# Kernel optimization log

Hardware: AMD Instinct MI355X
Metric: run time of the kernel (lower is better)

## Reference

```python
import jax, jax.numpy as jnp
import numpy as np

D_MODEL = 2048
N_HEADS = 16
GKV = 4
D_FF = 8192
D_HEAD = D_MODEL // N_HEADS
EPS = 1e-6


def rmsnorm(x, w):
    ms = jnp.mean(x * x, axis=-1, keepdims=True)
    return x * jax.lax.rsqrt(ms + EPS) * w


def attention(q, k, v, mask=None):
    # q: (B,Tq,H,d), k/v: (B,Tk,H,d)
    scale = 1.0 / jnp.sqrt(jnp.asarray(q.shape[-1], q.dtype))
    scores = jnp.einsum('bqhd,bkhd->bhqk', q, k) * scale
    if mask is not None:
        scores = scores + mask
    probs = jax.nn.softmax(scores, axis=-1)
    return jnp.einsum('bhqk,bkhd->bqhd', probs, v)


def setup_inputs() -> dict:
    key = jax.random.key(0)
    ks = jax.random.split(key, 12)
    B, T = 2, 2048
    s = 0.02
    return {
        'x': jax.random.normal(ks[0], (B, T, D_MODEL), jnp.float32),
        'k_ctx': jax.random.normal(ks[1], (B, T, GKV, D_HEAD), jnp.float32),
        'v_ctx': jax.random.normal(ks[2], (B, T, GKV, D_HEAD), jnp.float32),
        # cross-attn params (weights stored as (in, out); y = x @ W)
        'wq': jax.random.normal(ks[3], (D_MODEL, D_MODEL), jnp.float32) * s,
        'wo_cross': jax.random.normal(ks[4], (D_MODEL, D_MODEL), jnp.float32) * s,
        'norm_q_w': jnp.ones((D_MODEL,), jnp.float32),
        # self-attn params
        'wqkv': jax.random.normal(ks[5], (D_MODEL, 3 * D_MODEL), jnp.float32) * s,
        'wo_self': jax.random.normal(ks[6], (D_MODEL, D_MODEL), jnp.float32) * s,
        'norm_qkv_w': jnp.ones((D_MODEL,), jnp.float32),
        # FFN params (bias=False in FeedForward)
        'ffn_w1': jax.random.normal(ks[7], (D_MODEL, D_FF), jnp.float32) * s,
        'ffn_w2': jax.random.normal(ks[8], (D_FF, D_MODEL), jnp.float32) * s,
        'ffn_norm_w': jnp.ones((D_MODEL,), jnp.float32),
    }


def reference(x, k_ctx, v_ctx, wq, wo_cross, norm_q_w, wqkv, wo_self,
              norm_qkv_w, ffn_w1, ffn_w2, ffn_norm_w):
    B, T, D = x.shape
    repeat = N_HEADS // GKV

    # ---- cross attention (GQA) ----
    q = (rmsnorm(x, norm_q_w) @ wq).reshape(B, T, N_HEADS, D_HEAD)
    k = jnp.repeat(k_ctx, repeat, axis=2)  # (B,Tk,H,d), matches repeat_interleave
    v = jnp.repeat(v_ctx, repeat, axis=2)
    ctx = attention(q, k, v, mask=None).reshape(B, T, D)
    x = x + ctx @ wo_cross

    # ---- causal self attention ----
    xn = rmsnorm(x, norm_qkv_w)
    qkv = xn @ wqkv
    qs, ks_, vs = jnp.split(qkv, 3, axis=-1)
    qs = qs.reshape(B, T, N_HEADS, D_HEAD)
    ks_ = ks_.reshape(B, T, N_HEADS, D_HEAD)
    vs = vs.reshape(B, T, N_HEADS, D_HEAD)
    causal_mask = jnp.triu(jnp.full((T, T), -jnp.inf, x.dtype), k=1)[None, None]
    ctx2 = attention(qs, ks_, vs, mask=causal_mask).reshape(B, T, D)
    x = x + ctx2 @ wo_self

    # ---- FFN (SiLU) ----
    h = rmsnorm(x, ffn_norm_w)
    y = jax.nn.silu(h @ ffn_w1) @ ffn_w2
    return x + y
```

## Files before the change

kernel.cpp:

```cpp
#include <hip/hip_runtime.h>
#include <math.h>

typedef unsigned short u16;
typedef __attribute__((ext_vector_type(4))) u16 u16x4;
typedef __attribute__((ext_vector_type(8))) u16 u16x8;
typedef __attribute__((ext_vector_type(8))) __bf16 bf16x8;
typedef __attribute__((ext_vector_type(4))) float f32x4;
typedef __attribute__((ext_vector_type(16))) float f32x16;
typedef __attribute__((ext_vector_type(4))) unsigned u32x4;

#define D_MODEL 2048
#define SEQ 2048
#define BATCH 2
#define NH 16
#define HD 128
#define DFF 8192
#define ROWS (BATCH * SEQ)

__device__ __forceinline__ u16 f2bf(float f) {
  union { float f; unsigned u; } v; v.f = f;
  unsigned r = v.u + 0x7FFFu + ((v.u >> 16) & 1u);
  return (u16)(r >> 16);
}
__device__ __forceinline__ u16 to_bf16(float f) { return f2bf(f); }
__device__ __forceinline__ u16 to_bf16(u16 v) { return v; }

__device__ __forceinline__ f32x4 mfma16(u16x8 a, u16x8 b, f32x4 c) {
  return __builtin_amdgcn_mfma_f32_16x16x32_bf16(
      __builtin_bit_cast(bf16x8, a), __builtin_bit_cast(bf16x8, b), c, 0, 0, 0);
}
__device__ __forceinline__ f32x16 mfma32(u16x8 a, u16x8 b, f32x16 c) {
  return __builtin_amdgcn_mfma_f32_32x32x16_bf16(
      __builtin_bit_cast(bf16x8, a), __builtin_bit_cast(bf16x8, b), c, 0, 0, 0);
}

__device__ __forceinline__ void gll16(const void* g, void* l) {
  __builtin_amdgcn_global_load_lds(
      (const __attribute__((address_space(1))) void*)g,
      (__attribute__((address_space(3))) void*)l, 16, 0, 0);
}

__global__ __launch_bounds__(256) void cast_kernel(const float* __restrict__ in,
                                                   u16* __restrict__ out, int n8) {
  int i = blockIdx.x * 256 + threadIdx.x;
  if (i >= n8) return;
  const float4* p = (const float4*)in + (size_t)i * 2;
  float4 a = p[0], b = p[1];
  u16x8 o;
  o[0] = f2bf(a.x); o[1] = f2bf(a.y); o[2] = f2bf(a.z); o[3] = f2bf(a.w);
  o[4] = f2bf(b.x); o[5] = f2bf(b.y); o[6] = f2bf(b.z); o[7] = f2bf(b.w);
  *((u16x8*)out + i) = o;
}

__global__ __launch_bounds__(256) void cast_transpose_kernel(
    const float* __restrict__ in, u16* __restrict__ out, int K, int N) {
  __shared__ float tile[64][65];
  int n0 = blockIdx.x * 64, k0 = blockIdx.y * 64;
  int tx = threadIdx.x & 63, ty = threadIdx.x >> 6;
#pragma unroll
  for (int i = 0; i < 64; i += 4)
    tile[ty + i][tx] = in[(size_t)(k0 + ty + i) * N + n0 + tx];
  __syncthreads();
#pragma unroll
  for (int i = 0; i < 64; i += 4)
    out[(size_t)(n0 + ty + i) * K + k0 + tx] = f2bf(tile[tx][ty + i]);
}

template <typename ST>
__global__ __launch_bounds__(256) void build_vt_kernel(
    const ST* __restrict__ src, u16* __restrict__ dst, int HZ,
    size_t src_b_stride, size_t src_h_stride, int src_tok_stride) {
  __shared__ u16 tl[64][72];
  int z = blockIdx.z, zb = z / HZ, zh = z % HZ;
  const ST* s = src + (size_t)zb * src_b_stride + (size_t)zh * src_h_stride;
  int t0 = blockIdx.x * 64, d0 = blockIdx.y * 64;
  int rr = threadIdx.x >> 4, cc = (threadIdx.x & 15) * 4;
#pragma unroll
  for (int pp = 0; pp < 4; ++pp) {
    int t = pp * 16 + rr;
    const ST* sp = s + (size_t)(t0 + t) * src_tok_stride + d0 + cc;
#pragma unroll
    for (int j = 0; j < 4; ++j) tl[t][cc + j] = to_bf16(sp[j]);
  }
  __syncthreads();
  u16* dp = dst + (size_t)z * HD * SEQ;
#pragma unroll
  for (int pp = 0; pp < 4; ++pp) {
    int d = pp * 16 + rr;
    u16x4 w;
#pragma unroll
    for (int j = 0; j < 4; ++j) w[j] = tl[cc + j][d];
    *(u16x4*)(dp + (size_t)(d0 + d) * SEQ + t0 + cc) = w;
  }
}

__global__ __launch_bounds__(256) void rmsnorm_kernel(const float* __restrict__ x,
                                                      const float* __restrict__ w,
                                                      u16* __restrict__ out) {
  __shared__ float red[4];
  int row = blockIdx.x, t = threadIdx.x;
  const float4* xr = (const float4*)(x + (size_t)row * D_MODEL);
  float4 a = xr[t * 2], b = xr[t * 2 + 1];
  float ss = a.x * a.x + a.y * a.y + a.z * a.z + a.w * a.w +
             b.x * b.x + b.y * b.y + b.z * b.z + b.w * b.w;
#pragma unroll
  for (int m = 1; m < 64; m <<= 1) ss += __shfl_xor(ss, m, 64);
  if ((t & 63) == 0) red[t >> 6] = ss;
  __syncthreads();
  float tot = red[0] + red[1] + red[2] + red[3];
  float sc = rsqrtf(tot * (1.0f / D_MODEL) + 1e-6f);
  const float4* wr = (const float4*)w;
  float4 wa = wr[t * 2], wb = wr[t * 2 + 1];
  u16x8 o;
  o[0] = f2bf(a.x * sc * wa.x); o[1] = f2bf(a.y * sc * wa.y);
  o[2] = f2bf(a.z * sc * wa.z); o[3] = f2bf(a.w * sc * wa.w);
  o[4] = f2bf(b.x * sc * wb.x); o[5] = f2bf(b.y * sc * wb.y);
  o[6] = f2bf(b.z * sc * wb.z); o[7] = f2bf(b.w * sc * wb.w);
  *((u16x8*)(out + (size_t)row * D_MODEL) + t) = o;
}

template <int MODE>
__global__ __launch_bounds__(256) void combine_kernel(
    const float* __restrict__ p0, const float* __restrict__ p1,
    const float* __restrict__ res, void* __restrict__ outv, int n4) {
  int i = blockIdx.x * 256 + threadIdx.x;
  if (i >= n4) return;
  float4 a = ((const float4*)p0)[i];
  float4 b = ((const float4*)p1)[i];
  if (MODE == 1) {
    float4 r = ((const float4*)res)[i];
    float4 o;
    o.x = r.x + a.x + b.x; o.y = r.y + a.y + b.y;
    o.z = r.z + a.z + b.z; o.w = r.w + a.w + b.w;
    ((float4*)outv)[i] = o;
  } else {
    u16x4 o;
    o[0] = f2bf(a.x + b.x); o[1] = f2bf(a.y + b.y);
    o[2] = f2bf(a.z + b.z); o[3] = f2bf(a.w + b.w);
    ((u16x4*)outv)[i] = o;
  }
}

#define GPHASE(T, P, VM, ISSUE)                                                \
  {                                                                            \
    if (ISSUE) issue_half(4 * (T) + (P) + 4);                                  \
    asm volatile("s_waitcnt vmcnt(" #VM ")" ::: "memory");                     \
    __builtin_amdgcn_sched_barrier(0);                                         \
    __builtin_amdgcn_s_barrier();                                              \
    if (((P) & 1) == 0) {                                                      \
      const u16* SA = S + (((((T) & 1) << 2) | (((P) >> 1) << 1)) << 13);      \
      const u16* SB = SA + 8192;                                               \
      _Pragma("unroll") for (int m = 0; m < 8; ++m) {                          \
        int row = wm * 128 + m * 16 + r16;                                     \
        aF[m] = *(const u16x8*)(SA + row * 32 + ((kg ^ ((row >> 1) & 3)) << 3)); \
      }                                                                        \
      _Pragma("unroll") for (int n = 0; n < 4; ++n) {                          \
        int row = wn * 64 + n * 16 + r16;                                      \
        bF[n] = *(const u16x8*)(SB + row * 32 + ((kg ^ ((row >> 1) & 3)) << 3)); \
      }                                                                        \
    }                                                                          \
    __builtin_amdgcn_s_setprio(1);                                             \
    _Pragma("unroll") for (int m = 0; m < 8; ++m) {                            \
      acc[m][2 * ((P) & 1)] = mfma16(aF[m], bF[2 * ((P) & 1)], acc[m][2 * ((P) & 1)]); \
      acc[m][2 * ((P) & 1) + 1] =                                              \
          mfma16(aF[m], bF[2 * ((P) & 1) + 1], acc[m][2 * ((P) & 1) + 1]);     \
    }                                                                          \
    __builtin_amdgcn_s_setprio(0);                                             \
    __builtin_amdgcn_s_barrier();                                              \
  }

template <int EPI, int SPLIT>
__global__ __launch_bounds__(512, 1) void gemm256_kernel(
    const u16* __restrict__ A, const u16* __restrict__ Bt, void* __restrict__ Cv,
    float* __restrict__ Cv2, const float* __restrict__ res, int N, int K) {
  __shared__ __align__(16) u16 S[8 * 8192];
  const int tid = threadIdx.x, lane = tid & 63, wave = tid >> 6;
  const int wm = wave >> 2, wn = wave & 3;
  const int r16 = lane & 15, kg = lane >> 4;
  const int cols = N >> 8;
  const int cpx = gridDim.x >> 3;
  const int bid = blockIdx.x;
  const int swz = (bid & 7) * cpx + (bid >> 3);
  const int tiles = gridDim.x / SPLIT;
  const int tile = swz % tiles, kslice = swz / tiles;
  const int bm = (tile / cols) * 256, bn = (tile % cols) * 256;
  const int Ksub = K / SPLIT;
  const int koff = kslice * Ksub;
  const int nt = Ksub >> 6;

  auto issue_half = [&](int h) {
    int p = h & 3, t = h >> 2;
    const u16* src = (p & 1) ? (Bt + (size_t)bn * K) : (A + (size_t)bm * K);
    int kbase = koff + t * 64 + (p >> 1) * 32;
    u16* ldst = S + ((((t & 1) << 2) | p) << 13);
#pragma unroll
    for (int i = 0; i < 2; ++i) {
      int c = i * 512 + tid;
      int row = c >> 2, ch = c & 3;
      int kc = ch ^ ((row >> 1) & 3);
      gll16(src + (size_t)row * K + kbase + kc * 8, ldst + c * 8);
    }
  };

  u16x8 aF[8], bF[4];
  f32x4 acc[8][4] = {};

  issue_half(0); issue_half(1); issue_half(2); issue_half(3);
  for (int t = 0; t < nt - 1; ++t) {
    GPHASE(t, 0, 6, true);
    GPHASE(t, 1, 6, true);
    GPHASE(t, 2, 6, true);
    GPHASE(t, 3, 6, true);
  }
  {
    const int t = nt - 1;
    GPHASE(t, 0, 4, false);
    GPHASE(t, 1, 4, false);
    GPHASE(t, 2, 0, false);
    GPHASE(t, 3, 0, false);
  }

  float* Pp = (EPI == 3) ? (kslice ? Cv2 : (float*)Cv) : nullptr;
#pragma unroll
  for (int m = 0; m < 8; ++m) {
    int r0 = bm + wm * 128 + m * 16 + kg * 4;
#pragma unroll
    for (int n = 0; n < 4; ++n) {
      int cc = bn + wn * 64 + n * 16 + r16;
#pragma unroll
      for (int r = 0; r < 4; ++r) {
        size_t idx = (size_t)(r0 + r) * N + cc;
        float v = acc[m][n][r];
        if (EPI == 3) {
          Pp[idx] = v;
        } else if (EPI == 1) {
          ((float*)Cv)[idx] = res[idx] + v;
        } else if (EPI == 0) {
          ((u16*)Cv)[idx] = f2bf(v);
        } else {
          float s = v / (1.0f + __expf(-v));
          ((u16*)Cv)[idx] = f2bf(s);
        }
      }
    }
  }
}

#define NPH2(T, P, VM, ISSUE)                                                  \
  {                                                                            \
    if (ISSUE) issue_pair(2 * (T) + (P) + 1);                                  \
    asm volatile("s_waitcnt vmcnt(" #VM ")" ::: "memory");                     \
    __builtin_amdgcn_sched_barrier(0);                                         \
    __builtin_amdgcn_s_barrier();                                              \
    const u16* SA = S + (((2 * (T) + (P)) & 1) * 12288);                       \
    const u16* SB = SA + 8192;                                                 \
    u16x8 aF[4], bF[4];                                                        \
    _Pragma("unroll") for (int m = 0; m < 4; ++m) {                            \
      int row = wm * 64 + m * 16 + r16;                                        \
      aF[m] = *(const u16x8*)(SA + row * 32 + ((kg ^ ((row >> 1) & 3)) << 3)); \
    }                                                                          \
    _Pragma("unroll") for (int n = 0; n < 4; ++n) {                            \
      int row = wn * 64 + n * 16 + r16;                                        \
      bF[n] = *(const u16x8*)(SB + row * 32 + ((kg ^ ((row >> 1) & 3)) << 3)); \
    }                                                                          \
    __builtin_amdgcn_s_setprio(1);                                             \
    _Pragma("unroll") for (int m = 0; m < 4; ++m)                              \
      _Pragma("unroll") for (int n = 0; n < 4; ++n)                            \
        acc[m][n] = mfma16(aF[m], bF[n], acc[m][n]);                           \
    __builtin_amdgcn_s_setprio(0);                                             \
    __builtin_amdgcn_s_barrier();                                              \
  }

template <int EPI>
__global__ __launch_bounds__(512, 4) void gemm_n128_kernel(
    const u16* __restrict__ A, const u16* __restrict__ Bt, void* __restrict__ Cv,
    const float* __restrict__ res, u16* __restrict__ vt, int N, int K) {
  __shared__ __align__(16) u16 S[2 * 12288];
  const int tid = threadIdx.x, lane = tid & 63, wave = tid >> 6;
  const int wm = wave >> 1, wn = wave & 1;
  const int r16 = lane & 15, kg = lane >> 4;
  const int cols = N >> 7;
  const int cpx = gridDim.x >> 3;
  const int bid = blockIdx.x;
  const int swz = (bid & 7) * cpx + (bid >> 3);
  const int bm = (swz / cols) * 256, bn = (swz % cols) * 128;
  const int nt = K >> 6;

  auto issue_pair = [&](int g) {
    int p = g & 1, t = g >> 1;
    int kbase = t * 64 + p * 32;
    u16* reg = S + ((g & 1) * 12288);
#pragma unroll
    for (int i = 0; i < 2; ++i) {
      int c = i * 512 + tid;
      int row = c >> 2, ch = c & 3;
      int kc = ch ^ ((row >> 1) & 3);
      gll16(A + (size_t)(bm + row) * K + kbase + kc * 8, reg + c * 8);
    }
    {
      int row = tid >> 2, ch = tid & 3;
      int kc = ch ^ ((row >> 1) & 3);
      gll16(Bt + (size_t)(bn + row) * K + kbase + kc * 8, reg + 8192 + tid * 8);
    }
  };

  f32x4 acc[4][4] = {};

  issue_pair(0);
  for (int t = 0; t < nt - 1; ++t) {
    NPH2(t, 0, 3, true);
    NPH2(t, 1, 3, true);
  }
  NPH2(nt - 1, 0, 3, true);
  NPH2(nt - 1, 1, 0, false);

  const bool vmode = (EPI == 4) && (bn >= 4096);
#pragma unroll
  for (int m = 0; m < 4; ++m) {
    int r0 = bm + wm * 64 + m * 16 + kg * 4;
#pragma unroll
    for (int n = 0; n < 4; ++n) {
      int cc = bn + wn * 64 + n * 16 + r16;
      if (vmode) {
        int c2 = cc - 4096;
        int z = (r0 >> 11) * NH + (c2 >> 7);
        int d = c2 & 127;
        int t0 = r0 & (SEQ - 1);
        u16x4 w;
#pragma unroll
        for (int r = 0; r < 4; ++r) w[r] = f2bf(acc[m][n][r]);
        *(u16x4*)(vt + ((size_t)z * HD + d) * SEQ + t0) = w;
      } else {
#pragma unroll
        for (int r = 0; r < 4; ++r) {
          size_t idx = (size_t)(r0 + r) * N + cc;
          float v = acc[m][n][r];
          if (EPI == 1) {
            ((float*)Cv)[idx] = res[idx] + v;
          } else {
            ((u16*)Cv)[idx] = f2bf(v);
          }
        }
      }
    }
  }
}

template <bool CAUSAL, bool SELF>
__global__ __launch_bounds__(512, 2) void attn2_kernel(
    const u16* __restrict__ qp, const u16* __restrict__ kp,
    const u16* __restrict__ vtp, u16* __restrict__ outp) {
  __shared__ __align__(16) u16 Kl[2 * 64 * 128];
  __shared__ __align__(16) u16 Vl[2 * 128 * 64];
  const int tid = threadIdx.x, lane = tid & 63, wave = tid >> 6;
  const int lo = lane & 31, hi = lane >> 5;
  const int qt = blockIdx.x, bh = blockIdx.y, b = bh >> 4, h = bh & 15;
  const int qw0 = qt * 256 + wave * 32;
  const int qg = qw0 + lo;
  const size_t qstr = SELF ? 6144 : 2048;
  const size_t kstr = SELF ? 6144 : 512;
  const u16* qbase = qp + ((size_t)b * SEQ + qg) * qstr + h * HD;
  const u16* kbase = kp + (size_t)b * SEQ * kstr + (SELF ? (2048 + h * HD) : ((h >> 2) * HD));
  const u16* vbase = vtp + (size_t)(SELF ? (b * NH + h) : (b * 4 + (h >> 2))) * HD * SEQ;

  u16x8 qf[8];
#pragma unroll
  for (int dc = 0; dc < 8; ++dc) qf[dc] = *(const u16x8*)(qbase + dc * 16 + hi * 8);

  f32x16 o[4] = {};
  float m_run = -3e38f, l_run = 0.f;
  const int ntiles = CAUSAL ? qt * 4 + 4 : SEQ / 64;
  const float scale = 0.088388347648318447f;
  const float defer_thr = 90.50966799187809f;

  auto stage = [&](int kt, int buf) {
#pragma unroll
    for (int i = 0; i < 2; ++i) {
      int c = i * 512 + tid;
      int krow = c >> 4, ks = c & 15;
      gll16(kbase + (size_t)(kt * 64 + krow) * kstr + ((ks ^ (krow & 15)) * 8),
            Kl + (size_t)buf * 8192 + (size_t)c * 8);
      int vd = c >> 3, vs = c & 7;
      gll16(vbase + (size_t)vd * SEQ + kt * 64 + ((vs ^ (vd & 7)) * 8),
            Vl + (size_t)buf * 8192 + (size_t)c * 8);
    }
  };

  stage(0, 0);
  stage(1, 1);

  for (int kt = 0; kt < ntiles; ++kt) {
    if (kt + 1 < ntiles) {
      asm volatile("s_waitcnt vmcnt(4)" ::: "memory");
    } else {
      asm volatile("s_waitcnt vmcnt(0)" ::: "memory");
    }
    __builtin_amdgcn_sched_barrier(0);
    __syncthreads();
    const u16* Kb = Kl + (size_t)(kt & 1) * 8192;
    const u16* Vb = Vl + (size_t)(kt & 1) * 8192;

    if (!(CAUSAL && kt * 64 > qw0 + 31)) {
      f32x16 s01[2] = {};
#pragma unroll
      for (int k2 = 0; k2 < 2; ++k2) {
        int key = k2 * 32 + lo;
#pragma unroll
        for (int mf = 0; mf < 8; ++mf) {
          int dc = mf * 2 + hi;
          u16x8 kf = *(const u16x8*)(Kb + key * 128 + ((dc ^ (key & 15)) * 8));
          s01[k2] = mfma32(kf, qf[mf], s01[k2]);
        }
      }

      float sv[32];
      float pm = -3e38f;
#pragma unroll
      for (int k2 = 0; k2 < 2; ++k2)
#pragma unroll
        for (int r = 0; r < 16; ++r) {
          float v = s01[k2][r];
          if (CAUSAL) {
            int key = kt * 64 + k2 * 32 + (r & 3) + 8 * (r >> 2) + 4 * hi;
            if (key > qg) v = -3e38f;
          }
          sv[k2 * 16 + r] = v;
          pm = fmaxf(pm, v);
        }
      pm = fmaxf(pm, __shfl_xor(pm, 32, 64));

      const bool defer = __all(pm - m_run <= defer_thr);
      float mn = defer ? m_run : fmaxf(m_run, pm);
      float corr = defer ? 1.0f : __expf((m_run - mn) * scale);
      m_run = mn;

      float ps = 0.f;
      u16x8 pf[4];
#pragma unroll
      for (int k2 = 0; k2 < 2; ++k2)
#pragma unroll
        for (int hf = 0; hf < 2; ++hf) {
          float p8[8];
#pragma unroll
          for (int j = 0; j < 8; ++j) {
            p8[j] = __expf((sv[k2 * 16 + hf * 8 + j] - mn) * scale);
            ps += p8[j];
          }
          unsigned w0, w1, w2, w3;
          asm("v_cvt_pk_bf16_f32 %0, %1, %2" : "=v"(w0) : "v"(p8[0]), "v"(p8[1]));
          asm("v_cvt_pk_bf16_f32 %0, %1, %2" : "=v"(w1) : "v"(p8[2]), "v"(p8[3]));
          asm("v_cvt_pk_bf16_f32 %0, %1, %2" : "=v"(w2) : "v"(p8[4]), "v"(p8[5]));
          asm("v_cvt_pk_bf16_f32 %0, %1, %2" : "=v"(w3) : "v"(p8[6]), "v"(p8[7]));
          asm("v_permlane32_swap_b32 %0, %1" : "+v"(w0), "+v"(w2));
          asm("v_permlane32_swap_b32 %0, %1" : "+v"(w1), "+v"(w3));
          u32x4 fr; fr[0] = w0; fr[1] = w1; fr[2] = w2; fr[3] = w3;
          pf[k2 * 2 + hf] = __builtin_bit_cast(u16x8, fr);
        }
      ps += __shfl_xor(ps, 32, 64);

      if (defer) {
        l_run += ps;
      } else {
        l_run = l_run * corr + ps;
#pragma unroll
        for (int mb = 0; mb < 4; ++mb)
#pragma unroll
          for (int r = 0; r < 16; ++r) o[mb][r] *= corr;
      }

#pragma unroll
      for (int kc = 0; kc < 4; ++kc) {
        int vcs = kc * 2 + hi;
#pragma unroll
        for (int mb = 0; mb < 4; ++mb) {
          int d = mb * 32 + lo;
          u16x8 vf = *(const u16x8*)(Vb + d * 64 + ((vcs ^ (d & 7)) * 8));
          o[mb] = mfma32(vf, pf[kc], o[mb]);
        }
      }
    }

    __syncthreads();
    if (kt + 2 < ntiles) stage(kt + 2, kt & 1);
  }

  float inv = 1.0f / l_run;
  u16* ob = outp + ((size_t)b * SEQ + qg) * D_MODEL + h * HD + 4 * hi;
#pragma unroll
  for (int mb = 0; mb < 4; ++mb)
#pragma unroll
    for (int rq = 0; rq < 4; ++rq) {
      u16x4 w;
#pragma unroll
      for (int j = 0; j < 4; ++j) w[j] = f2bf(o[mb][rq * 4 + j] * inv);
      *(u16x4*)(ob + mb * 32 + rq * 8) = w;
    }
}

extern "C" void kernel_launch(void* const* d_in, const int* in_sizes, int n_in,
                              void* d_out, int out_size, void* d_ws, size_t ws_size,
                              hipStream_t stream) {
  const float* x          = (const float*)d_in[0];
  const float* k_ctx      = (const float*)d_in[1];
  const float* v_ctx      = (const float*)d_in[2];
  const float* wq         = (const float*)d_in[3];
  const float* wo_cross   = (const float*)d_in[4];
  const float* norm_q_w   = (const float*)d_in[5];
  const float* wqkv       = (const float*)d_in[6];
  const float* wo_self    = (const float*)d_in[7];
  const float* norm_qkv_w = (const float*)d_in[8];
  const float* ffn_w1     = (const float*)d_in[9];
  const float* ffn_w2     = (const float*)d_in[10];
  const float* ffn_norm_w = (const float*)d_in[11];
  float* out = (float*)d_out;

  char* ws = (char*)d_ws;
  size_t off = 0;
  auto alloc_u16 = [&](size_t n) { u16* p = (u16*)(ws + off); off += n * 2; return p; };
  auto alloc_f32 = [&](size_t n) { float* p = (float*)(ws + off); off += n * 4; return p; };
  u16* wq_bf   = alloc_u16((size_t)2048 * 2048);
  u16* woc_bf  = alloc_u16((size_t)2048 * 2048);
  u16* wqkv_bf = alloc_u16((size_t)2048 * 6144);
  u16* wos_bf  = alloc_u16((size_t)2048 * 2048);
  u16* w1_bf   = alloc_u16((size_t)2048 * 8192);
  u16* w2_bf   = alloc_u16((size_t)8192 * 2048);
  u16* xn_bf   = alloc_u16((size_t)ROWS * 2048);
  u16* qkv_bf  = alloc_u16((size_t)ROWS * 6144);
  u16* attn_bf = alloc_u16((size_t)ROWS * 2048);
  float* x1    = alloc_f32((size_t)ROWS * 2048);
  float* x2    = alloc_f32((size_t)ROWS * 2048);
  u16* q_bf    = qkv_bf;
  u16* h1_bf   = qkv_bf;
  u16* kc_bf   = (u16*)x2;
  u16* vt_ctx  = kc_bf + (size_t)BATCH * SEQ * 4 * HD;
  u16* vt_self = (u16*)x2;
  const int n4 = ROWS * 2048 / 4;

  auto castT = [&](const float* src, u16* dst, int K, int N) {
    cast_transpose_kernel<<<dim3(N / 64, K / 64), 256, 0, stream>>>(src, dst, K, N);
  };
  castT(wq, wq_bf, 2048, 2048);
  castT(wo_cross, woc_bf, 2048, 2048);
  castT(wqkv, wqkv_bf, 2048, 6144);
  castT(wo_self, wos_bf, 2048, 2048);
  castT(ffn_w1, w1_bf, 2048, 8192);
  castT(ffn_w2, w2_bf, 8192, 2048);
  {
    int n8 = (int)((size_t)BATCH * SEQ * 4 * HD / 8);
    cast_kernel<<<dim3((n8 + 255) / 256), dim3(256), 0, stream>>>(k_ctx, kc_bf, n8);
  }
  build_vt_kernel<float><<<dim3(SEQ / 64, HD / 64, BATCH * 4), 256, 0, stream>>>(
      v_ctx, vt_ctx, 4, (size_t)SEQ * 512, (size_t)HD, 512);

  rmsnorm_kernel<<<ROWS, 256, 0, stream>>>(x, norm_q_w, xn_bf);
  gemm_n128_kernel<0><<<dim3((ROWS / 256) * (2048 / 128)), 512, 0, stream>>>(
      xn_bf, wq_bf, q_bf, nullptr, nullptr, 2048, 2048);
  attn2_kernel<false, false><<<dim3(SEQ / 256, BATCH * NH), 512, 0, stream>>>(
      q_bf, kc_bf, vt_ctx, attn_bf);
  gemm_n128_kernel<1><<<dim3((ROWS / 256) * (2048 / 128)), 512, 0, stream>>>(
      attn_bf, woc_bf, x1, x, nullptr, 2048, 2048);

  rmsnorm_kernel<<<ROWS, 256, 0, stream>>>(x1, norm_qkv_w, xn_bf);
  gemm_n128_kernel<4><<<dim3((ROWS / 256) * (6144 / 128)), 512, 0, stream>>>(
      xn_bf, wqkv_bf, qkv_bf, nullptr, vt_self, 6144, 2048);
  attn2_kernel<true, true><<<dim3(SEQ / 256, BATCH * NH), 512, 0, stream>>>(
      qkv_bf, qkv_bf, vt_self, attn_bf);
  gemm_n128_kernel<1><<<dim3((ROWS / 256) * (2048 / 128)), 512, 0, stream>>>(
      attn_bf, wos_bf, x2, x1, nullptr, 2048, 2048);

  rmsnorm_kernel<<<ROWS, 256, 0, stream>>>(x2, ffn_norm_w, xn_bf);
  gemm256_kernel<2, 1><<<dim3((ROWS / 256) * (8192 / 256)), 512, 0, stream>>>(
      xn_bf, w1_bf, h1_bf, nullptr, nullptr, 8192, 2048);
  gemm256_kernel<3, 2><<<dim3(256), 512, 0, stream>>>(
      h1_bf, w2_bf, out, x1, nullptr, 2048, 8192);
  combine_kernel<1><<<dim3((n4 + 255) / 256), 256, 0, stream>>>(
      out, x1, x2, out, n4);
}
```

Before: 828.5 us.

## Batch weight cast-transposes into one launch and prefetch GEMM fragments earlier

The six per-weight cast-transpose launches are merged into one kernel that picks its weight by block index, and it now uses float4 loads and u16x4 stores. The 256-tile GEMM main loop is restructured so the LDS fragments for the next half-step are loaded right after the current MFMAs instead of at the start of the next phase. The vmcnt waits are retuned to match, so LDS reads overlap with waiting on global loads. This adds register pressure and tighter barrier/wait correctness requirements.

```diff
diff --git a/kernel.cpp b/kernel.cpp
--- a/kernel.cpp
+++ b/kernel.cpp
@@ -52,18 +52,41 @@
   *((u16x8*)out + i) = o;
 }
 
-__global__ __launch_bounds__(256) void cast_transpose_kernel(
-    const float* __restrict__ in, u16* __restrict__ out, int K, int N) {
-  __shared__ float tile[64][65];
-  int n0 = blockIdx.x * 64, k0 = blockIdx.y * 64;
-  int tx = threadIdx.x & 63, ty = threadIdx.x >> 6;
-#pragma unroll
-  for (int i = 0; i < 64; i += 4)
-    tile[ty + i][tx] = in[(size_t)(k0 + ty + i) * N + n0 + tx];
+struct WTArgs {
+  const float* src[6];
+  u16* dst[6];
+  int K[6], N[6];
+  int start[7];
+};
+
+__global__ __launch_bounds__(256) void cast_transpose_all(WTArgs a) {
+  __shared__ float tile[64][69];
+  int b = blockIdx.x;
+  int wi = 0;
+#pragma unroll
+  for (int i = 0; i < 6; ++i)
+    if (b >= a.start[i + 1]) wi = i + 1;
+  const float* src = a.src[wi];
+  u16* dst = a.dst[wi];
+  int K = a.K[wi], N = a.N[wi];
+  int t = b - a.start[wi];
+  int cols = N >> 6;
+  int n0 = (t % cols) * 64, k0 = (t / cols) * 64;
+  int rr = threadIdx.x >> 4, cc = (threadIdx.x & 15) * 4;
+#pragma unroll
+  for (int pp = 0; pp < 4; ++pp) {
+    int kk = pp * 16 + rr;
+    *(float4*)&tile[kk][cc] = *(const float4*)(src + (size_t)(k0 + kk) * N + n0 + cc);
+  }
   __syncthreads();
 #pragma unroll
-  for (int i = 0; i < 64; i += 4)
-    out[(size_t)(n0 + ty + i) * K + k0 + tx] = f2bf(tile[tx][ty + i]);
+  for (int pp = 0; pp < 4; ++pp) {
+    int d = pp * 16 + rr;
+    u16x4 w;
+#pragma unroll
+    for (int j = 0; j < 4; ++j) w[j] = f2bf(tile[cc + j][d]);
+    *(u16x4*)(dst + (size_t)(n0 + d) * K + k0 + cc) = w;
+  }
 }
 
 template <typename ST>
@@ -141,31 +164,54 @@
   }
 }
 
-#define GPHASE(T, P, VM, ISSUE)                                                \
+#define LOADFRAGS(BASE)                                                        \
+  {                                                                            \
+    const u16* SA = S + (BASE);                                                \
+    const u16* SB = SA + 8192;                                                 \
+    _Pragma("unroll") for (int m = 0; m < 8; ++m) {                            \
+      int row = wm * 128 + m * 16 + r16;                                       \
+      aF[m] = *(const u16x8*)(SA + row * 32 + ((kg ^ ((row >> 1) & 3)) << 3)); \
+    }                                                                          \
+    _Pragma("unroll") for (int n = 0; n < 4; ++n) {                            \
+      int row = wn * 64 + n * 16 + r16;                                        \
+      bF[n] = *(const u16x8*)(SB + row * 32 + ((kg ^ ((row >> 1) & 3)) << 3)); \
+    }                                                                          \
+  }
+
+#define MFMA_HALF(HH)                                                          \
+  __builtin_amdgcn_s_setprio(1);                                               \
+  _Pragma("unroll") for (int m = 0; m < 8; ++m) {                              \
+    acc[m][2 * (HH)] = mfma16(aF[m], bF[2 * (HH)], acc[m][2 * (HH)]);          \
+    acc[m][2 * (HH) + 1] =                                                     \
+        mfma16(aF[m], bF[2 * (HH) + 1], acc[m][2 * (HH) + 1]);                 \
+  }                                                                            \
+  __builtin_amdgcn_s_setprio(0);
+
+#define GPH_E(T, P, VM, ISSUE, FIRST)                                          \
   {                                                                            \
     if (ISSUE) issue_half(4 * (T) + (P) + 4);                                  \
     asm volatile("s_waitcnt vmcnt(" #VM ")" ::: "memory");                     \
     __builtin_amdgcn_sched_barrier(0);                                         \
     __builtin_amdgcn_s_barrier();                                              \
-    if (((P) & 1) == 0) {                                                      \
-      const u16* SA = S + (((((T) & 1) << 2) | (((P) >> 1) << 1)) << 13);      \
-      const u16* SB = SA + 8192;                                               \
-      _Pragma("unroll") for (int m = 0; m < 8; ++m) {                          \
-        int row = wm * 128 + m * 16 + r16;                                     \
-        aF[m] = *(const u16x8*)(SA + row * 32 + ((kg ^ ((row >> 1) & 3)) << 3)); \
-      }                                                                        \
-      _Pragma("unroll") for (int n = 0; n < 4; ++n) {                          \
-        int row = wn * 64 + n * 16 + r16;                                      \
-        bF[n] = *(const u16x8*)(SB + row * 32 + ((kg ^ ((row >> 1) & 3)) << 3)); \
+    if (FIRST) LOADFRAGS((((((T) & 1) << 2) | (P)) << 13));                    \
+    MFMA_HALF(0)                                                               \
+    __builtin_amdgcn_s_barrier();                                              \
+  }
+
+#define GPH_O(T, P, VM, ISSUE, PF)                                             \
+  {                                                                            \
+    if (ISSUE) issue_half(4 * (T) + (P) + 4);                                  \
+    asm volatile("s_waitcnt vmcnt(" #VM ")" ::: "memory");                     \
+    __builtin_amdgcn_sched_barrier(0);                                         \
+    __builtin_amdgcn_s_barrier();                                              \
+    MFMA_HALF(1)                                                               \
+    if (PF) {                                                                  \
+      if ((P) == 1) {                                                          \
+        LOADFRAGS((((((T) & 1) << 2) | 2) << 13));                             \
+      } else {                                                                 \
+        LOADFRAGS(((((T) + 1) & 1) << 2) << 13);                               \
       }                                                                        \
     }                                                                          \
-    __builtin_amdgcn_s_setprio(1);                                             \
-    _Pragma("unroll") for (int m = 0; m < 8; ++m) {                            \
-      acc[m][2 * ((P) & 1)] = mfma16(aF[m], bF[2 * ((P) & 1)], acc[m][2 * ((P) & 1)]); \
-      acc[m][2 * ((P) & 1) + 1] =                                              \
-          mfma16(aF[m], bF[2 * ((P) & 1) + 1], acc[m][2 * ((P) & 1) + 1]);     \
-    }                                                                          \
-    __builtin_amdgcn_s_setprio(0);                                             \
     __builtin_amdgcn_s_barrier();                                              \
   }
 
@@ -206,18 +252,22 @@
   f32x4 acc[8][4] = {};
 
   issue_half(0); issue_half(1); issue_half(2); issue_half(3);
-  for (int t = 0; t < nt - 1; ++t) {
-    GPHASE(t, 0, 6, true);
-    GPHASE(t, 1, 6, true);
-    GPHASE(t, 2, 6, true);
-    GPHASE(t, 3, 6, true);
+  GPH_E(0, 0, 6, true, true);
+  GPH_O(0, 1, 4, true, true);
+  GPH_E(0, 2, 6, true, false);
+  GPH_O(0, 3, 4, true, true);
+  for (int t = 1; t < nt - 1; ++t) {
+    GPH_E(t, 0, 6, true, false);
+    GPH_O(t, 1, 4, true, true);
+    GPH_E(t, 2, 6, true, false);
+    GPH_O(t, 3, 4, true, true);
   }
   {
     const int t = nt - 1;
-    GPHASE(t, 0, 4, false);
-    GPHASE(t, 1, 4, false);
-    GPHASE(t, 2, 0, false);
-    GPHASE(t, 3, 0, false);
+    GPH_E(t, 0, 6, false, false);
+    GPH_O(t, 1, 0, false, true);
+    GPH_E(t, 2, 0, false, false);
+    GPH_O(t, 3, 0, false, false);
   }
 
   float* Pp = (EPI == 3) ? (kslice ? Cv2 : (float*)Cv) : nullptr;
@@ -536,15 +586,21 @@
   u16* vt_self = (u16*)x2;
   const int n4 = ROWS * 2048 / 4;
 
-  auto castT = [&](const float* src, u16* dst, int K, int N) {
-    cast_transpose_kernel<<<dim3(N / 64, K / 64), 256, 0, stream>>>(src, dst, K, N);
-  };
-  castT(wq, wq_bf, 2048, 2048);
-  castT(wo_cross, woc_bf, 2048, 2048);
-  castT(wqkv, wqkv_bf, 2048, 6144);
-  castT(wo_self, wos_bf, 2048, 2048);
-  castT(ffn_w1, w1_bf, 2048, 8192);
-  castT(ffn_w2, w2_bf, 8192, 2048);
+  {
+    WTArgs wt;
+    const float* s6[6] = {wq, wo_cross, wqkv, wo_self, ffn_w1, ffn_w2};
+    u16* d6[6] = {wq_bf, woc_bf, wqkv_bf, wos_bf, w1_bf, w2_bf};
+    int K6[6] = {2048, 2048, 2048, 2048, 2048, 8192};
+    int N6[6] = {2048, 2048, 6144, 2048, 8192, 2048};
+    int s = 0;
+    wt.start[0] = 0;
+    for (int i = 0; i < 6; ++i) {
+      wt.src[i] = s6[i]; wt.dst[i] = d6[i]; wt.K[i] = K6[i]; wt.N[i] = N6[i];
+      s += (N6[i] >> 6) * (K6[i] >> 6);
+      wt.start[i + 1] = s;
+    }
+    cast_transpose_all<<<dim3(s), 256, 0, stream>>>(wt);
+  }
   {
     int n8 = (int)((size_t)BATCH * SEQ * 4 * HD / 8);
     cast_kernel<<<dim3((n8 + 255) / 256), dim3(256), 0, stream>>>(k_ctx, kc_bf, n8);
```

Measured after the change: 814.8 us. Within noise of the previous version (-1.6%).
